# Optimization experiments

Hardware: AMD Instinct MI355X
Metric: run time of the kernel (lower is better)

## Reference

```python
import jax, jax.numpy as jnp
import numpy as np
import math

D_MODEL = 768
NUM_HEADS = 8
D_ATT = D_MODEL // NUM_HEADS


def _pos_encoding(S):
    # pe: [S, d_model] sinusoidal, scaled by d_model**-0.5, reshaped to [h, S, d_att]
    position = jnp.arange(S, dtype=jnp.float32)[:, None]                      # [S,1]
    div_term = jnp.exp(jnp.arange(0, D_MODEL, 2, dtype=jnp.float32)
                       * (-math.log(10000.0) / D_MODEL))                      # [d_model/2]
    pe = jnp.zeros((S, D_MODEL), dtype=jnp.float32)
    pe = pe.at[:, 0::2].set(jnp.sin(position * div_term))
    pe = pe.at[:, 1::2].set(jnp.cos(position * div_term))
    pe = pe * (D_MODEL ** -0.5)
    return pe.reshape(S, NUM_HEADS, D_ATT).transpose(1, 0, 2)                 # [h,S,d]


def setup_inputs() -> dict:
    key = jax.random.key(0)
    k1, k2 = jax.random.split(key)
    B, S = 16, 4096
    src = jax.random.normal(k1, (B, S, D_MODEL), dtype=jnp.float32)
    src_key_padding_mask = jnp.zeros((B, S), dtype=bool)  # all valid
    query = jax.random.normal(k2, (NUM_HEADS, D_ATT), dtype=jnp.float32) * (D_ATT ** -0.5)
    return {"src": src, "src_key_padding_mask": src_key_padding_mask, "query": query}


def reference(src, src_key_padding_mask, query):
    B, S, C = src.shape
    key = src.reshape(B, S, NUM_HEADS, D_ATT).transpose(0, 2, 1, 3)          # [B,h,S,d]
    val = key + _pos_encoding(S)[None]                                        # [B,h,S,d]
    scores = jnp.einsum('hd,bhsd->bhs', query, key)                           # [B,h,S]
    scores = jnp.where(src_key_padding_mask[:, None, :], -jnp.inf, scores)
    weights = jax.nn.softmax(scores, axis=-1)                                 # [B,h,S]
    pooled = jnp.einsum('bhsd,bhs->bhd', val, weights)                        # [B,h,d]
    return pooled.reshape(B, NUM_HEADS * D_ATT)                               # [B,C]
```

## Files before the change

kernel.cpp:

```cpp
#include <hip/hip_runtime.h>
#include <math.h>

namespace {
constexpr int kB = 16;
constexpr int kS = 4096;
constexpr int kH = 8;
constexpr int kD = 96;
constexpr int kDM = 768;
constexpr int kNChunk = 16;
constexpr int kCS = kS / kNChunk;
constexpr int kRPI = 32;
constexpr int kIters = kCS / kRPI;
constexpr float kPeScale = 0.03608439182435161f;
constexpr float kNegLog = -9.210340371976184f / 768.0f;
}

__global__ __launch_bounds__(256)
void attn_partial_kernel(const float* __restrict__ src,
                         const unsigned char* __restrict__ mask,
                         const float* __restrict__ query,
                         float* __restrict__ wsO,
                         float* __restrict__ wsL)
{
    const int blk = blockIdx.x;
    const int chunk = blk % kNChunk;
    const int bh = blk / kNChunk;
    const int b = bh / kH;
    const int h = bh % kH;
    const int t = (int)threadIdx.x;
    const int j = t & 7;
    const int r = t >> 3;
    const int lane = t & 63;
    const int wave = t >> 6;

    const float* qh = query + h * kD + 4 * j;
    const float4 q0 = *(const float4*)(qh);
    const float4 q1 = *(const float4*)(qh + 32);
    const float4 q2 = *(const float4*)(qh + 64);

    const int cbase = h * kD + 4 * j;
    const float f0 = __expf(kNegLog * (float)(cbase));
    const float f1 = __expf(kNegLog * (float)(cbase + 2));
    const float f2 = __expf(kNegLog * (float)(cbase + 32));
    const float f3 = __expf(kNegLog * (float)(cbase + 34));
    const float f4 = __expf(kNegLog * (float)(cbase + 64));
    const float f5 = __expf(kNegLog * (float)(cbase + 66));

    const float s0f = (float)(chunk * kCS + r);
    float sn0, cs0, sn1, cs1, sn2, cs2, sn3, cs3, sn4, cs4, sn5, cs5;
    __sincosf(s0f * f0, &sn0, &cs0);
    __sincosf(s0f * f1, &sn1, &cs1);
    __sincosf(s0f * f2, &sn2, &cs2);
    __sincosf(s0f * f3, &sn3, &cs3);
    __sincosf(s0f * f4, &sn4, &cs4);
    __sincosf(s0f * f5, &sn5, &cs5);
    float dsn0, dcs0, dsn1, dcs1, dsn2, dcs2, dsn3, dcs3, dsn4, dcs4, dsn5, dcs5;
    __sincosf((float)kRPI * f0, &dsn0, &dcs0);
    __sincosf((float)kRPI * f1, &dsn1, &dcs1);
    __sincosf((float)kRPI * f2, &dsn2, &dcs2);
    __sincosf((float)kRPI * f3, &dsn3, &dcs3);
    __sincosf((float)kRPI * f4, &dsn4, &dcs4);
    __sincosf((float)kRPI * f5, &dsn5, &dcs5);

    float l = 0.0f;
    float o[12];
#pragma unroll
    for (int k = 0; k < 12; ++k) o[k] = 0.0f;

    const float* baseT = src + ((size_t)b * kS + (size_t)(chunk * kCS + r)) * kDM
                       + h * kD + 4 * j;
    const unsigned char* mbase = mask + (size_t)b * kS + chunk * kCS + r;

    float4 x0 = *(const float4*)(baseT);
    float4 x1 = *(const float4*)(baseT + 32);
    float4 x2 = *(const float4*)(baseT + 64);
    unsigned char mk = mbase[0];

#pragma unroll
    for (int it = 0; it < kIters; ++it) {
        float4 nx0 = {}, nx1 = {}, nx2 = {};
        unsigned char nmk = 0;
        if (it + 1 < kIters) {
            const float* np = baseT + (size_t)(it + 1) * kRPI * kDM;
            nx0 = *(const float4*)(np);
            nx1 = *(const float4*)(np + 32);
            nx2 = *(const float4*)(np + 64);
            nmk = mbase[(it + 1) * kRPI];
        }

        float pd = x0.x * q0.x + x0.y * q0.y + x0.z * q0.z + x0.w * q0.w
                 + x1.x * q1.x + x1.y * q1.y + x1.z * q1.z + x1.w * q1.w
                 + x2.x * q2.x + x2.y * q2.y + x2.z * q2.z + x2.w * q2.w;
        pd += __shfl_xor(pd, 1, 8);
        pd += __shfl_xor(pd, 2, 8);
        pd += __shfl_xor(pd, 4, 8);

        const float w = mk ? 0.0f : __expf(pd);
        l += w;

        o[0]  = fmaf(w, fmaf(sn0, kPeScale, x0.x), o[0]);
        o[1]  = fmaf(w, fmaf(cs0, kPeScale, x0.y), o[1]);
        o[2]  = fmaf(w, fmaf(sn1, kPeScale, x0.z), o[2]);
        o[3]  = fmaf(w, fmaf(cs1, kPeScale, x0.w), o[3]);
        o[4]  = fmaf(w, fmaf(sn2, kPeScale, x1.x), o[4]);
        o[5]  = fmaf(w, fmaf(cs2, kPeScale, x1.y), o[5]);
        o[6]  = fmaf(w, fmaf(sn3, kPeScale, x1.z), o[6]);
        o[7]  = fmaf(w, fmaf(cs3, kPeScale, x1.w), o[7]);
        o[8]  = fmaf(w, fmaf(sn4, kPeScale, x2.x), o[8]);
        o[9]  = fmaf(w, fmaf(cs4, kPeScale, x2.y), o[9]);
        o[10] = fmaf(w, fmaf(sn5, kPeScale, x2.z), o[10]);
        o[11] = fmaf(w, fmaf(cs5, kPeScale, x2.w), o[11]);

        float tns, tnc;
        tns = fmaf(sn0, dcs0, cs0 * dsn0); tnc = fmaf(cs0, dcs0, -sn0 * dsn0); sn0 = tns; cs0 = tnc;
        tns = fmaf(sn1, dcs1, cs1 * dsn1); tnc = fmaf(cs1, dcs1, -sn1 * dsn1); sn1 = tns; cs1 = tnc;
        tns = fmaf(sn2, dcs2, cs2 * dsn2); tnc = fmaf(cs2, dcs2, -sn2 * dsn2); sn2 = tns; cs2 = tnc;
        tns = fmaf(sn3, dcs3, cs3 * dsn3); tnc = fmaf(cs3, dcs3, -sn3 * dsn3); sn3 = tns; cs3 = tnc;
        tns = fmaf(sn4, dcs4, cs4 * dsn4); tnc = fmaf(cs4, dcs4, -sn4 * dsn4); sn4 = tns; cs4 = tnc;
        tns = fmaf(sn5, dcs5, cs5 * dsn5); tnc = fmaf(cs5, dcs5, -sn5 * dsn5); sn5 = tns; cs5 = tnc;

        x0 = nx0; x1 = nx1; x2 = nx2; mk = nmk;
    }

    __shared__ float ssum[4];
    __shared__ float osh[4][8][12];

    float lv = (j == 0) ? l : 0.0f;
#pragma unroll
    for (int msk = 32; msk >= 1; msk >>= 1) lv += __shfl_xor(lv, msk, 64);
    if (lane == 0) ssum[wave] = lv;

#pragma unroll
    for (int k = 0; k < 12; ++k) {
        float v = o[k];
        v += __shfl_xor(v, 8, 64);
        v += __shfl_xor(v, 16, 64);
        v += __shfl_xor(v, 32, 64);
        o[k] = v;
    }
    if (lane < 8) {
#pragma unroll
        for (int k = 0; k < 12; ++k) osh[wave][lane][k] = o[k];
    }
    __syncthreads();

    const int pidx = bh * kNChunk + chunk;
    if (t < kD) {
        const int kk = t >> 5;
        const int jj = (t & 31) >> 2;
        const int qq = t & 3;
        const int idx = kk * 4 + qq;
        wsO[(size_t)pidx * kD + t] = osh[0][jj][idx] + osh[1][jj][idx]
                                   + osh[2][jj][idx] + osh[3][jj][idx];
    }
    if (t == 0) {
        wsL[pidx] = ssum[0] + ssum[1] + ssum[2] + ssum[3];
    }
}

__global__ __launch_bounds__(128)
void attn_combine_kernel(const float* __restrict__ wsO,
                         const float* __restrict__ wsL,
                         float* __restrict__ out)
{
    const int bh = (int)blockIdx.x;
    const int t = (int)threadIdx.x;

    float L = 0.0f;
#pragma unroll
    for (int c = 0; c < kNChunk; ++c) L += wsL[bh * kNChunk + c];

    if (t < kD) {
        float Od = 0.0f;
#pragma unroll
        for (int c = 0; c < kNChunk; ++c)
            Od += wsO[(size_t)(bh * kNChunk + c) * kD + t];
        out[(size_t)bh * kD + t] = Od / L;
    }
}

extern "C" void kernel_launch(void* const* d_in, const int* in_sizes, int n_in,
                              void* d_out, int out_size, void* d_ws, size_t ws_size,
                              hipStream_t stream)
{
    const float* src = (const float*)d_in[0];
    const unsigned char* mask = (const unsigned char*)d_in[1];
    const float* query = (const float*)d_in[2];
    float* out = (float*)d_out;

    float* wsO = (float*)d_ws;
    float* wsL = wsO + (size_t)kB * kH * kNChunk * kD;

    hipLaunchKernelGGL(attn_partial_kernel,
                       dim3(kB * kH * kNChunk), dim3(256), 0, stream,
                       src, mask, query, wsO, wsL);
    hipLaunchKernelGGL(attn_combine_kernel,
                       dim3(kB * kH), dim3(128), 0, stream,
                       wsO, wsL, out);
}
```

Before: 276.1 us.

## Split positional-encoding term into separate weight-times-PE reduction kernel

```diff
diff --git a/kernel.cpp b/kernel.cpp
--- a/kernel.cpp
+++ b/kernel.cpp
@@ -11,22 +11,26 @@
 constexpr int kCS = kS / kNChunk;
 constexpr int kRPI = 32;
 constexpr int kIters = kCS / kRPI;
+constexpr int kNSC2 = 32;
+constexpr int kS2 = kS / kNSC2;
 constexpr float kPeScale = 0.03608439182435161f;
 constexpr float kNegLog = -9.210340371976184f / 768.0f;
-}
-
-__global__ __launch_bounds__(256)
-void attn_partial_kernel(const float* __restrict__ src,
-                         const unsigned char* __restrict__ mask,
-                         const float* __restrict__ query,
-                         float* __restrict__ wsO,
-                         float* __restrict__ wsL)
+constexpr float kHalfPi = 1.5707963267948966f;
+}
+
+__global__ __launch_bounds__(256, 8)
+void attn_pass1_kernel(const float* __restrict__ src,
+                       const unsigned char* __restrict__ mask,
+                       const float* __restrict__ query,
+                       float* __restrict__ wsO,
+                       float* __restrict__ wsL,
+                       float* __restrict__ wsW)
 {
     const int blk = blockIdx.x;
-    const int chunk = blk % kNChunk;
-    const int bh = blk / kNChunk;
-    const int b = bh / kH;
-    const int h = bh % kH;
+    const int chunk = blk & (kNChunk - 1);
+    const int bh = blk >> 4;
+    const int b = bh >> 3;
+    const int h = bh & 7;
     const int t = (int)threadIdx.x;
     const int j = t & 7;
     const int r = t >> 3;
@@ -38,55 +42,23 @@
     const float4 q1 = *(const float4*)(qh + 32);
     const float4 q2 = *(const float4*)(qh + 64);
 
-    const int cbase = h * kD + 4 * j;
-    const float f0 = __expf(kNegLog * (float)(cbase));
-    const float f1 = __expf(kNegLog * (float)(cbase + 2));
-    const float f2 = __expf(kNegLog * (float)(cbase + 32));
-    const float f3 = __expf(kNegLog * (float)(cbase + 34));
-    const float f4 = __expf(kNegLog * (float)(cbase + 64));
-    const float f5 = __expf(kNegLog * (float)(cbase + 66));
-
-    const float s0f = (float)(chunk * kCS + r);
-    float sn0, cs0, sn1, cs1, sn2, cs2, sn3, cs3, sn4, cs4, sn5, cs5;
-    __sincosf(s0f * f0, &sn0, &cs0);
-    __sincosf(s0f * f1, &sn1, &cs1);
-    __sincosf(s0f * f2, &sn2, &cs2);
-    __sincosf(s0f * f3, &sn3, &cs3);
-    __sincosf(s0f * f4, &sn4, &cs4);
-    __sincosf(s0f * f5, &sn5, &cs5);
-    float dsn0, dcs0, dsn1, dcs1, dsn2, dcs2, dsn3, dcs3, dsn4, dcs4, dsn5, dcs5;
-    __sincosf((float)kRPI * f0, &dsn0, &dcs0);
-    __sincosf((float)kRPI * f1, &dsn1, &dcs1);
-    __sincosf((float)kRPI * f2, &dsn2, &dcs2);
-    __sincosf((float)kRPI * f3, &dsn3, &dcs3);
-    __sincosf((float)kRPI * f4, &dsn4, &dcs4);
-    __sincosf((float)kRPI * f5, &dsn5, &dcs5);
-
     float l = 0.0f;
     float o[12];
 #pragma unroll
     for (int k = 0; k < 12; ++k) o[k] = 0.0f;
 
-    const float* baseT = src + ((size_t)b * kS + (size_t)(chunk * kCS + r)) * kDM
-                       + h * kD + 4 * j;
-    const unsigned char* mbase = mask + (size_t)b * kS + chunk * kCS + r;
-
-    float4 x0 = *(const float4*)(baseT);
-    float4 x1 = *(const float4*)(baseT + 32);
-    float4 x2 = *(const float4*)(baseT + 64);
-    unsigned char mk = mbase[0];
-
-#pragma unroll
+    const int s0 = chunk * kCS + r;
+    const float* baseT = src + ((size_t)b * kS + s0) * kDM + h * kD + 4 * j;
+    const unsigned char* mbase = mask + (size_t)b * kS + s0;
+    float* wbase = wsW + (size_t)bh * kS + s0;
+
+#pragma unroll 1
     for (int it = 0; it < kIters; ++it) {
-        float4 nx0 = {}, nx1 = {}, nx2 = {};
-        unsigned char nmk = 0;
-        if (it + 1 < kIters) {
-            const float* np = baseT + (size_t)(it + 1) * kRPI * kDM;
-            nx0 = *(const float4*)(np);
-            nx1 = *(const float4*)(np + 32);
-            nx2 = *(const float4*)(np + 64);
-            nmk = mbase[(it + 1) * kRPI];
-        }
+        const float* rp = baseT + (size_t)(it * kRPI) * kDM;
+        const float4 x0 = *(const float4*)(rp);
+        const float4 x1 = *(const float4*)(rp + 32);
+        const float4 x2 = *(const float4*)(rp + 64);
+        const unsigned char mk = mbase[it * kRPI];
 
         float pd = x0.x * q0.x + x0.y * q0.y + x0.z * q0.z + x0.w * q0.w
                  + x1.x * q1.x + x1.y * q1.y + x1.z * q1.z + x1.w * q1.w
@@ -98,28 +70,20 @@
         const float w = mk ? 0.0f : __expf(pd);
         l += w;
 
-        o[0]  = fmaf(w, fmaf(sn0, kPeScale, x0.x), o[0]);
-        o[1]  = fmaf(w, fmaf(cs0, kPeScale, x0.y), o[1]);
-        o[2]  = fmaf(w, fmaf(sn1, kPeScale, x0.z), o[2]);
-        o[3]  = fmaf(w, fmaf(cs1, kPeScale, x0.w), o[3]);
-        o[4]  = fmaf(w, fmaf(sn2, kPeScale, x1.x), o[4]);
-        o[5]  = fmaf(w, fmaf(cs2, kPeScale, x1.y), o[5]);
-        o[6]  = fmaf(w, fmaf(sn3, kPeScale, x1.z), o[6]);
-        o[7]  = fmaf(w, fmaf(cs3, kPeScale, x1.w), o[7]);
-        o[8]  = fmaf(w, fmaf(sn4, kPeScale, x2.x), o[8]);
-        o[9]  = fmaf(w, fmaf(cs4, kPeScale, x2.y), o[9]);
-        o[10] = fmaf(w, fmaf(sn5, kPeScale, x2.z), o[10]);
-        o[11] = fmaf(w, fmaf(cs5, kPeScale, x2.w), o[11]);
-
-        float tns, tnc;
-        tns = fmaf(sn0, dcs0, cs0 * dsn0); tnc = fmaf(cs0, dcs0, -sn0 * dsn0); sn0 = tns; cs0 = tnc;
-        tns = fmaf(sn1, dcs1, cs1 * dsn1); tnc = fmaf(cs1, dcs1, -sn1 * dsn1); sn1 = tns; cs1 = tnc;
-        tns = fmaf(sn2, dcs2, cs2 * dsn2); tnc = fmaf(cs2, dcs2, -sn2 * dsn2); sn2 = tns; cs2 = tnc;
-        tns = fmaf(sn3, dcs3, cs3 * dsn3); tnc = fmaf(cs3, dcs3, -sn3 * dsn3); sn3 = tns; cs3 = tnc;
-        tns = fmaf(sn4, dcs4, cs4 * dsn4); tnc = fmaf(cs4, dcs4, -sn4 * dsn4); sn4 = tns; cs4 = tnc;
-        tns = fmaf(sn5, dcs5, cs5 * dsn5); tnc = fmaf(cs5, dcs5, -sn5 * dsn5); sn5 = tns; cs5 = tnc;
-
-        x0 = nx0; x1 = nx1; x2 = nx2; mk = nmk;
+        o[0]  = fmaf(w, x0.x, o[0]);
+        o[1]  = fmaf(w, x0.y, o[1]);
+        o[2]  = fmaf(w, x0.z, o[2]);
+        o[3]  = fmaf(w, x0.w, o[3]);
+        o[4]  = fmaf(w, x1.x, o[4]);
+        o[5]  = fmaf(w, x1.y, o[5]);
+        o[6]  = fmaf(w, x1.z, o[6]);
+        o[7]  = fmaf(w, x1.w, o[7]);
+        o[8]  = fmaf(w, x2.x, o[8]);
+        o[9]  = fmaf(w, x2.y, o[9]);
+        o[10] = fmaf(w, x2.z, o[10]);
+        o[11] = fmaf(w, x2.w, o[11]);
+
+        if (j == 0) wbase[it * kRPI] = w;
     }
 
     __shared__ float ssum[4];
@@ -159,8 +123,39 @@
 }
 
 __global__ __launch_bounds__(128)
+void attn_pe_kernel(const float* __restrict__ wsW, float* __restrict__ wsP)
+{
+    const int blk = (int)blockIdx.x;
+    const int sc = blk & (kNSC2 - 1);
+    const int bh = blk >> 5;
+    const int h = bh & 7;
+    const int c = (int)threadIdx.x;
+    if (c >= kD) return;
+
+    const float f = __expf(kNegLog * (float)(h * kD + (c & ~1)));
+    const int s0 = sc * kS2;
+    float sn, cs;
+    __sincosf((float)s0 * f + ((c & 1) ? kHalfPi : 0.0f), &sn, &cs);
+    float ds, dc;
+    __sincosf(f, &ds, &dc);
+
+    const float* wp = wsW + (size_t)bh * kS + s0;
+    float acc = 0.0f;
+#pragma unroll 4
+    for (int i = 0; i < kS2; ++i) {
+        const float w = wp[i];
+        acc = fmaf(w, sn, acc);
+        const float ns = fmaf(sn, dc, cs * ds);
+        const float nc = fmaf(cs, dc, -sn * ds);
+        sn = ns; cs = nc;
+    }
+    wsP[(size_t)blk * kD + c] = acc * kPeScale;
+}
+
+__global__ __launch_bounds__(128)
 void attn_combine_kernel(const float* __restrict__ wsO,
                          const float* __restrict__ wsL,
+                         const float* __restrict__ wsP,
                          float* __restrict__ out)
 {
     const int bh = (int)blockIdx.x;
@@ -168,14 +163,17 @@
 
     float L = 0.0f;
 #pragma unroll
-    for (int c = 0; c < kNChunk; ++c) L += wsL[bh * kNChunk + c];
+    for (int k = 0; k < kNChunk; ++k) L += wsL[bh * kNChunk + k];
 
     if (t < kD) {
-        float Od = 0.0f;
-#pragma unroll
-        for (int c = 0; c < kNChunk; ++c)
-            Od += wsO[(size_t)(bh * kNChunk + c) * kD + t];
-        out[(size_t)bh * kD + t] = Od / L;
+        float acc = 0.0f;
+#pragma unroll
+        for (int k = 0; k < kNChunk; ++k)
+            acc += wsO[(size_t)(bh * kNChunk + k) * kD + t];
+#pragma unroll
+        for (int k = 0; k < kNSC2; ++k)
+            acc += wsP[(size_t)(bh * kNSC2 + k) * kD + t];
+        out[(size_t)bh * kD + t] = acc / L;
     }
 }
 
@@ -190,11 +188,16 @@
 
     float* wsO = (float*)d_ws;
     float* wsL = wsO + (size_t)kB * kH * kNChunk * kD;
-
-    hipLaunchKernelGGL(attn_partial_kernel,
+    float* wsW = wsL + (size_t)kB * kH * kNChunk;
+    float* wsP = wsW + (size_t)kB * kH * kS;
+
+    hipLaunchKernelGGL(attn_pass1_kernel,
                        dim3(kB * kH * kNChunk), dim3(256), 0, stream,
-                       src, mask, query, wsO, wsL);
+                       src, mask, query, wsO, wsL, wsW);
+    hipLaunchKernelGGL(attn_pe_kernel,
+                       dim3(kB * kH * kNSC2), dim3(128), 0, stream,
+                       wsW, wsP);
     hipLaunchKernelGGL(attn_combine_kernel,
                        dim3(kB * kH), dim3(128), 0, stream,
-                       wsO, wsL, out);
-}
+                       wsO, wsL, wsP, out);
+}
```

New measurement: 292.1 us. +5.8%, slower.
